# Kernel optimization log

Measured on AMD Instinct MI355X. Metric: run time of the kernel, lower is better.

The kernel has to match this reference:

```python
import jax, jax.numpy as jnp
import numpy as np

N_E = 1024     # codebook size (n_e, nbooks=1)
E_DIM = 256    # embedding dim
BETA = 0.25
B, T = 16, 4096


def setup_inputs() -> dict:
    key = jax.random.key(0)
    k1, k2 = jax.random.split(key)
    z = jax.random.normal(k1, (B, T, E_DIM), dtype=jnp.float32)
    # matches torch init: uniform(-1/n_e_i, 1/n_e_i)
    codebook = jax.random.uniform(k2, (N_E, E_DIM), dtype=jnp.float32,
                                  minval=-1.0 / N_E, maxval=1.0 / N_E)
    return {"z": z, "codebook": codebook}


def reference(z, codebook):
    zf = z.reshape(-1, E_DIM)                                   # [N, d]
    dist = (jnp.sum(zf * zf, axis=1, keepdims=True)
            - 2.0 * (zf @ codebook.T)
            + jnp.sum(codebook * codebook, axis=1)[None, :])
    idx = jnp.argmin(dist, axis=1)                              # [N]
    # one-hot scatter + matmul == codebook gather
    z_q = codebook[idx].reshape(z.shape)                        # [B, T, d]
    loss = (jnp.mean((z_q - jax.lax.stop_gradient(z)) ** 2)
            + BETA * jnp.mean((z - jax.lax.stop_gradient(z_q)) ** 2))
    # straight-through estimator
    z_q_st = z + jax.lax.stop_gradient(z_q - z)
    indices = idx.reshape(z.shape[:-1] + (1,))                  # [B, T, 1]
    return z_q_st, loss, indices
```

## Files before the change

kernel.cpp:

```cpp
#include <hip/hip_runtime.h>
#include <hip/hip_bf16.h>
#include <math.h>

typedef __bf16 bf16x8 __attribute__((ext_vector_type(8)));
typedef float f32x4 __attribute__((ext_vector_type(4)));
typedef unsigned short u16x8 __attribute__((ext_vector_type(8)));

constexpr int EDIM = 256;
constexpr int NE = 1024;
constexpr int NROWS = 65536;
constexpr float BETA = 0.25f;

constexpr size_t A2T_OFF   = 0;
constexpr size_t A2T_SZ    = (size_t)512 * 16 * 8192;
constexpr size_t B2T_OFF   = A2T_OFF + A2T_SZ;
constexpr size_t B2T_SZ    = (size_t)8 * 16 * 8192;
constexpr size_t SZROW_OFF = B2T_OFF + B2T_SZ;
constexpr size_t SZABS_OFF = SZROW_OFF + 262144;
constexpr size_t CNORM_OFF = SZABS_OFF + 262144;
constexpr size_t BMAX_OFF  = CNORM_OFF + 4096;
constexpr size_t EMAX_OFF  = BMAX_OFF + 4096;
constexpr size_t CNT_OFF   = EMAX_OFF + 256;
constexpr size_t LIST_OFF  = CNT_OFF + 256;
constexpr size_t LPART_OFF = LIST_OFF + 262144;
constexpr size_t LP2_OFF   = LPART_OFF + 262144;
constexpr size_t WS_NEED   = LP2_OFF + 1024;

__device__ __forceinline__ unsigned short f32_to_bf16_rne(float f) {
    unsigned u = __float_as_uint(f);
    u += 0x7fffu + ((u >> 16) & 1u);
    return (unsigned short)(u >> 16);
}
__device__ __forceinline__ float bf16_to_f32(unsigned short h) {
    return __uint_as_float((unsigned)h << 16);
}

#define GLL16(g, l)                                                                   \
    __builtin_amdgcn_global_load_lds(                                                 \
        (const __attribute__((address_space(1))) unsigned int*)(g),                   \
        (__attribute__((address_space(3))) unsigned int*)(l), 16, 0, 0)

__global__ __launch_bounds__(64)
void p3_codebook(const float* __restrict__ cb, float* __restrict__ cnorm,
                 char* __restrict__ B2t, float* __restrict__ bmax) {
    __shared__ float xr[256];
    __shared__ float rres[16];
    __shared__ unsigned short ehi[256], elo[256];
    const int e = blockIdx.x, l = threadIdx.x;
    const float4 v = reinterpret_cast<const float4*>(cb + (size_t)e * EDIM)[l];
    *reinterpret_cast<float4*>(&xr[l * 4]) = v;
    float amax = fmaxf(fmaxf(fabsf(v.x), fabsf(v.y)), fmaxf(fabsf(v.z), fabsf(v.w)));
    #pragma unroll
    for (int off = 32; off; off >>= 1) amax = fmaxf(amax, __shfl_down(amax, off));
    __syncthreads();
    #pragma unroll
    for (int i = 0; i < 4; ++i) {
        const int idx = i * 64 + l;
        const float f = xr[idx];
        const unsigned short h = f32_to_bf16_rne(f);
        ehi[idx] = h;
        elo[idx] = f32_to_bf16_rne(f - bf16_to_f32(h));
    }
    if (l < 16) {
        const float* x = xr + (l >> 3) * 128;
        const int j = l & 7;
        float r = __fmul_rn(x[j], x[j]);
        for (int i = 8; i < 128; i += 8) r = __fadd_rn(r, __fmul_rn(x[i + j], x[i + j]));
        rres[l] = r;
    }
    __syncthreads();
    if (l == 0) {
        float h0 = __fadd_rn(__fadd_rn(__fadd_rn(rres[0], rres[1]), __fadd_rn(rres[2], rres[3])),
                             __fadd_rn(__fadd_rn(rres[4], rres[5]), __fadd_rn(rres[6], rres[7])));
        float h1 = __fadd_rn(__fadd_rn(__fadd_rn(rres[8], rres[9]), __fadd_rn(rres[10], rres[11])),
                             __fadd_rn(__fadd_rn(rres[12], rres[13]), __fadd_rn(rres[14], rres[15])));
        cnorm[e] = __fadd_rn(h0, h1);
        bmax[e] = amax;
    }
    {
        const int c = l >> 2, kgv = l & 3;
        const int colbase = ((c < 8) ? c * 32 : (c - 8) * 32) + kgv * 8;
        const unsigned short* src = (c < 8) ? ehi : elo;
        char* dst = B2t + ((((size_t)(e >> 7) * 16 + c) * 512 + (size_t)kgv * 128 + (e & 127)) * 16);
        *reinterpret_cast<uint4*>(dst) = *reinterpret_cast<const uint4*>(&src[colbase]);
    }
}

__global__ void k_emax(const float* __restrict__ bmax, float* __restrict__ emax, int* cnt) {
    __shared__ float red[256];
    if (threadIdx.x == 0) cnt[0] = 0;
    float m = 0.f;
    for (int i = threadIdx.x; i < NE; i += 256) m = fmaxf(m, bmax[i]);
    red[threadIdx.x] = m;
    __syncthreads();
    for (int h = 128; h; h >>= 1) {
        if (threadIdx.x < h) red[threadIdx.x] = fmaxf(red[threadIdx.x], red[threadIdx.x + h]);
        __syncthreads();
    }
    if (threadIdx.x == 0) emax[0] = red[0];
}

__global__ __launch_bounds__(256)
void p2_atile(const float* __restrict__ z, char* __restrict__ A2t,
              float* __restrict__ szrow, float* __restrict__ szabs) {
    __shared__ float t[64][260];
    __shared__ float ch[64][16];
    const int mt = blockIdx.x, h = blockIdx.y, tid = threadIdx.x;
    const int row0 = mt * 128 + h * 64;
    #pragma unroll
    for (int i = 0; i < 16; ++i) {
        const int fid = i * 256 + tid;
        const int r = fid >> 6, c4 = fid & 63;
        const float4 v = *reinterpret_cast<const float4*>(
            z + (size_t)(row0 + r) * EDIM + c4 * 4);
        *reinterpret_cast<float4*>(&t[r][c4 * 4]) = v;
    }
    __syncthreads();
    {
        const int r = tid >> 2, q = tid & 3;
        float asum = 0.f;
        for (int c = 0; c < 64; ++c) asum += fabsf(t[r][q * 64 + c]);
        asum += __shfl_xor(asum, 1);
        asum += __shfl_xor(asum, 2);
        #pragma unroll
        for (int cc = 0; cc < 4; ++cc) {
            const int chain = q * 4 + cc;
            const float* x = &t[r][(chain >> 3) * 128];
            const int j = chain & 7;
            float rr = __fmul_rn(x[j], x[j]);
            for (int i = 8; i < 128; i += 8) rr = __fadd_rn(rr, __fmul_rn(x[i + j], x[i + j]));
            ch[r][chain] = rr;
        }
        __syncthreads();
        if (q == 0) {
            const float* c0 = ch[r];
            const float h0 = __fadd_rn(__fadd_rn(__fadd_rn(c0[0], c0[1]), __fadd_rn(c0[2], c0[3])),
                                       __fadd_rn(__fadd_rn(c0[4], c0[5]), __fadd_rn(c0[6], c0[7])));
            const float h1 = __fadd_rn(__fadd_rn(__fadd_rn(c0[8], c0[9]), __fadd_rn(c0[10], c0[11])),
                                       __fadd_rn(__fadd_rn(c0[12], c0[13]), __fadd_rn(c0[14], c0[15])));
            szrow[row0 + r] = __fadd_rn(h0, h1);
            szabs[row0 + r] = asum;
        }
    }
    #pragma unroll
    for (int i = 0; i < 16; ++i) {
        const int sid = i * 256 + tid;
        const int ca = sid >> 8, kgv = (sid >> 6) & 3, rwl = sid & 63;
        const int cbase = ((ca < 8) ? ca : ca - 8) * 32 + kgv * 8;
        u16x8 out;
        #pragma unroll
        for (int j = 0; j < 8; ++j) {
            const float f = t[rwl][cbase + j];
            unsigned short h16 = f32_to_bf16_rne(f);
            if (ca >= 8) h16 = f32_to_bf16_rne(f - bf16_to_f32(h16));
            out[j] = h16;
        }
        char* dst = A2t + ((((size_t)mt * 16 + ca) * 512 + (size_t)kgv * 128 + (h * 64 + rwl)) * 16);
        *reinterpret_cast<u16x8*>(dst) = out;
    }
}

__global__ __launch_bounds__(256, 1)
void vq_main(const char* __restrict__ A2t, const char* __restrict__ B2t,
             const float* __restrict__ cnorm, const float* __restrict__ szrow,
             const float* __restrict__ szabs, const float* __restrict__ emaxp,
             const float* __restrict__ cb,
             float* __restrict__ idxf, int* __restrict__ cnt, int* __restrict__ list,
             float* __restrict__ zq, float* __restrict__ lpart) {
    constexpr int CNS = 131072;
    __shared__ char smem[135168] __attribute__((aligned(16)));
    float* cns = reinterpret_cast<float*>(smem + CNS);
    float (*ms1)[2] = reinterpret_cast<float(*)[2]>(smem);
    float (*ms2)[2] = reinterpret_cast<float(*)[2]>(smem + 1024);
    int   (*mi1)[2] = reinterpret_cast<int(*)[2]>(smem + 2048);
    int*  bidx      = reinterpret_cast<int*>(smem + 3072);

    const int tid = threadIdx.x;
    const int mtile = blockIdx.x;
    const size_t rowbase = (size_t)mtile * 128;
    const int l = tid & 63, wid = tid >> 6;
    const int kg = l >> 4, li = l & 15;
    const int wr = wid >> 1, wc = wid & 1;

    GLL16((const char*)cnorm + tid * 16, smem + CNS + tid * 16);
    const char* Ag = A2t + (size_t)mtile * 131072;
    #pragma unroll
    for (int i = 0; i < 32; ++i)
        GLL16(Ag + (i * 256 + tid) * 16, smem + (i * 256 + tid) * 16);
    asm volatile("s_waitcnt vmcnt(0)" ::: "memory");
    __syncthreads();

    int aoff[4], boff[4];
    #pragma unroll
    for (int f = 0; f < 4; ++f) {
        aoff[f] = kg * 2048 + (wr * 64 + f * 16 + li) * 16;
        boff[f] = kg * 2048 + (wc * 64 + f * 16 + li) * 16;
    }

    bf16x8 cAh[4], cAl[4], cB[4];
    #pragma unroll
    for (int f = 0; f < 4; ++f) {
        cAh[f] = *reinterpret_cast<const bf16x8*>(smem + 0 * 8192 + aoff[f]);
        cAl[f] = *reinterpret_cast<const bf16x8*>(smem + 8 * 8192 + aoff[f]);
        cB[f]  = *reinterpret_cast<const bf16x8*>(B2t + boff[f]);
    }

    float s1v[4][4], s2v[4][4];
    int i1v[4][4];
    #pragma unroll
    for (int a = 0; a < 4; ++a)
        #pragma unroll
        for (int b = 0; b < 4; ++b) { s1v[a][b] = 3.4e38f; s2v[a][b] = 3.4e38f; i1v[a][b] = 0; }

    for (int nt = 0; nt < 8; ++nt) {
        f32x4 acc[4][4];
        const f32x4 zf4 = {0.f, 0.f, 0.f, 0.f};
        #pragma unroll
        for (int a = 0; a < 4; ++a)
            #pragma unroll
            for (int b = 0; b < 4; ++b) acc[a][b] = zf4;

        #pragma unroll
        for (int j = 0; j < 16; ++j) {
            const int g = nt * 16 + j;
            bf16x8 nAh[4], nAl[4], nB[4];
            {
                const int jn = (j + 1) & 15;
                const char* gB = B2t + (size_t)(g + 1) * 8192;
                #pragma unroll
                for (int f = 0; f < 4; ++f)
                    nB[f] = *reinterpret_cast<const bf16x8*>(gB + boff[f]);
                if (jn < 8) {
                    #pragma unroll
                    for (int f = 0; f < 4; ++f) {
                        nAh[f] = *reinterpret_cast<const bf16x8*>(smem + jn * 8192 + aoff[f]);
                        nAl[f] = *reinterpret_cast<const bf16x8*>(smem + (8 + jn) * 8192 + aoff[f]);
                    }
                } else {
                    #pragma unroll
                    for (int f = 0; f < 4; ++f) {
                        nAh[f] = *reinterpret_cast<const bf16x8*>(smem + (jn - 8) * 8192 + aoff[f]);
                        nAl[f] = cAl[f];
                    }
                }
            }
            #pragma unroll
            for (int fm = 0; fm < 4; ++fm)
                #pragma unroll
                for (int fn = 0; fn < 4; ++fn)
                    acc[fm][fn] = __builtin_amdgcn_mfma_f32_16x16x32_bf16(cAh[fm], cB[fn], acc[fm][fn], 0, 0, 0);
            if (j < 8) {
                #pragma unroll
                for (int fm = 0; fm < 4; ++fm)
                    #pragma unroll
                    for (int fn = 0; fn < 4; ++fn)
                        acc[fm][fn] = __builtin_amdgcn_mfma_f32_16x16x32_bf16(cAl[fm], cB[fn], acc[fm][fn], 0, 0, 0);
            }
            #pragma unroll
            for (int f = 0; f < 4; ++f) { cAh[f] = nAh[f]; cAl[f] = nAl[f]; cB[f] = nB[f]; }
        }

        const int ntb = nt * 128;
        #pragma unroll
        for (int fn = 0; fn < 4; ++fn) {
            const int e = ntb + wc * 64 + fn * 16 + li;
            const float cn = cns[e];
            #pragma unroll
            for (int fm = 0; fm < 4; ++fm)
                #pragma unroll
                for (int r = 0; r < 4; ++r) {
                    const float s = cn - 2.0f * acc[fm][fn][r];
                    if (s < s1v[fm][r]) { s2v[fm][r] = s1v[fm][r]; s1v[fm][r] = s; i1v[fm][r] = e; }
                    else s2v[fm][r] = fminf(s2v[fm][r], s);
                }
        }
    }

    __syncthreads();

    #pragma unroll
    for (int fm = 0; fm < 4; ++fm)
        #pragma unroll
        for (int r = 0; r < 4; ++r) {
            float s1 = s1v[fm][r], s2 = s2v[fm][r];
            int i1 = i1v[fm][r];
            #pragma unroll
            for (int off = 1; off < 16; off <<= 1) {
                const float os1 = __shfl_xor(s1, off);
                const float os2 = __shfl_xor(s2, off);
                const int oi1 = __shfl_xor(i1, off);
                const bool take = (os1 < s1) || (os1 == s1 && oi1 < i1);
                const float loser = take ? s1 : os1;
                if (take) { s1 = os1; i1 = oi1; }
                s2 = fminf(fminf(s2, os2), loser);
            }
            if (li == 0) {
                const int rloc = wr * 64 + fm * 16 + (kg << 2) + r;
                ms1[rloc][wc] = s1; ms2[rloc][wc] = s2; mi1[rloc][wc] = i1;
            }
        }
    __syncthreads();

    if (tid < 128) {
        const float a1 = ms1[tid][0], b1 = ms1[tid][1];
        const float a2 = ms2[tid][0], b2 = ms2[tid][1];
        const int ai = mi1[tid][0], bi = mi1[tid][1];
        const bool take = (b1 < a1) || (b1 == a1 && bi < ai);
        const float s1 = take ? b1 : a1;
        const int i1 = take ? bi : ai;
        const float loser = take ? a1 : b1;
        const float s2 = fminf(fminf(a2, b2), loser);
        const int rowg = (int)rowbase + tid;
        const float szv = szrow[rowg], sab = szabs[rowg];
        const float M = 2.0e-4f * sab * emaxp[0] + ldexpf(1.0f, ilogbf(szv * 1.02f) - 23);
        idxf[rowg] = (float)i1;
        lpart[rowg] = s1 + szv;
        bidx[tid] = i1;
        if (s2 - s1 <= 2.0f * M) { const int p = atomicAdd(cnt, 1); list[p] = rowg; }
    }
    __syncthreads();

    {
        const float4* cb4 = reinterpret_cast<const float4*>(cb);
        float4* zq4 = reinterpret_cast<float4*>(zq);
        #pragma unroll 4
        for (int j = 0; j < 32; ++j) {
            const int rr = wid * 32 + j;
            const int e = bidx[rr];
            zq4[(rowbase + rr) * 64 + l] = cb4[(size_t)e * 64 + l];
        }
    }
}

__global__ __launch_bounds__(256)
void vq_rescan(const float* __restrict__ z, const float* __restrict__ cb,
               const float* __restrict__ cnorm, const float* __restrict__ szrow,
               const int* __restrict__ list, const int* __restrict__ cntp,
               float* __restrict__ idxf, float* __restrict__ zq, float* __restrict__ lpart) {
    __shared__ float zr[8][260];
    __shared__ float szs[8];
    __shared__ int rows_s[8];
    __shared__ float sred[256];
    __shared__ int ired[256];
    const int tid = threadIdx.x;
    const int n = cntp[0];
    const int groups = (n + 7) >> 3;
    for (int g = blockIdx.x; g < groups; g += gridDim.x) {
        if (tid < 8) {
            const int gi = g * 8 + tid;
            const int row = (gi < n) ? list[gi] : -1;
            rows_s[tid] = row;
            szs[tid] = (row >= 0) ? szrow[row] : 0.f;
        }
        __syncthreads();
        #pragma unroll
        for (int i = 0; i < 8; ++i) {
            const int sid = i * 256 + tid;
            const int rr = sid >> 8, k = sid & 255;
            if (rows_s[rr] >= 0) zr[rr][k] = z[(size_t)rows_s[rr] * EDIM + k];
        }
        __syncthreads();
        float bs[8];
        int bi[8];
        #pragma unroll
        for (int rr = 0; rr < 8; ++rr) { bs[rr] = 3.4e38f; bi[rr] = 0; }
        for (int q = 0; q < 4; ++q) {
            const int e = tid + q * 256;
            const float4* crow = reinterpret_cast<const float4*>(cb + (size_t)e * EDIM);
            float d[8];
            #pragma unroll
            for (int rr = 0; rr < 8; ++rr) d[rr] = 0.f;
            for (int k4 = 0; k4 < 64; ++k4) {
                const float4 c4 = crow[k4];
                #pragma unroll
                for (int rr = 0; rr < 8; ++rr) {
                    d[rr] = fmaf(zr[rr][k4 * 4 + 0], c4.x, d[rr]);
                    d[rr] = fmaf(zr[rr][k4 * 4 + 1], c4.y, d[rr]);
                    d[rr] = fmaf(zr[rr][k4 * 4 + 2], c4.z, d[rr]);
                    d[rr] = fmaf(zr[rr][k4 * 4 + 3], c4.w, d[rr]);
                }
            }
            const float cn = cnorm[e];
            #pragma unroll
            for (int rr = 0; rr < 8; ++rr) {
                const float b1 = __fadd_rn(szs[rr], __fmul_rn(-2.0f, d[rr]));
                const float s = __fadd_rn(b1, cn);
                if (s < bs[rr]) { bs[rr] = s; bi[rr] = e; }
            }
        }
        #pragma unroll
        for (int rr = 0; rr < 8; ++rr) {
            sred[tid] = bs[rr];
            ired[tid] = bi[rr];
            __syncthreads();
            for (int h = 128; h; h >>= 1) {
                if (tid < h) {
                    const float so = sred[tid + h];
                    const int io = ired[tid + h];
                    if (so < sred[tid] || (so == sred[tid] && io < ired[tid])) {
                        sred[tid] = so; ired[tid] = io;
                    }
                }
                __syncthreads();
            }
            if (rows_s[rr] >= 0) {
                const int best = ired[0];
                const int row = rows_s[rr];
                zq[(size_t)row * EDIM + tid] = cb[(size_t)best * EDIM + tid];
                if (tid == 0) { idxf[row] = (float)best; lpart[row] = sred[0]; }
            }
            __syncthreads();
        }
    }
}

__global__ void vq_loss1(const float* __restrict__ lpart, float* __restrict__ lp2) {
    __shared__ float red[256];
    const int t = threadIdx.x;
    red[t] = lpart[blockIdx.x * 256 + t];
    __syncthreads();
    for (int h = 128; h; h >>= 1) {
        if (t < h) red[t] += red[t + h];
        __syncthreads();
    }
    if (t == 0) lp2[blockIdx.x] = red[0];
}
__global__ void vq_loss2(const float* __restrict__ lp2, float* __restrict__ outloss) {
    __shared__ float red[256];
    const int t = threadIdx.x;
    red[t] = lp2[t];
    __syncthreads();
    for (int h = 128; h; h >>= 1) {
        if (t < h) red[t] += red[t + h];
        __syncthreads();
    }
    if (t == 0) outloss[0] = red[0] * ((1.0f + BETA) / 16777216.0f);
}

__device__ __forceinline__ float np_sum128_sq(const float* __restrict__ x) {
    float r[8];
    #pragma unroll
    for (int j = 0; j < 8; ++j) r[j] = __fmul_rn(x[j], x[j]);
    #pragma unroll
    for (int i = 8; i < 128; i += 8)
        #pragma unroll
        for (int j = 0; j < 8; ++j) r[j] = __fadd_rn(r[j], __fmul_rn(x[i + j], x[i + j]));
    return __fadd_rn(__fadd_rn(__fadd_rn(r[0], r[1]), __fadd_rn(r[2], r[3])),
                     __fadd_rn(__fadd_rn(r[4], r[5]), __fadd_rn(r[6], r[7])));
}
__global__ void fb_prep(const float* __restrict__ z, const float* __restrict__ cb,
                        float* __restrict__ szrow, float* __restrict__ cnorm) {
    int t = blockIdx.x * blockDim.x + threadIdx.x;
    if (t < NROWS) {
        const float* x = z + (size_t)t * EDIM;
        szrow[t] = __fadd_rn(np_sum128_sq(x), np_sum128_sq(x + 128));
    } else if (t < NROWS + NE) {
        const float* x = cb + (size_t)(t - NROWS) * EDIM;
        cnorm[t - NROWS] = __fadd_rn(np_sum128_sq(x), np_sum128_sq(x + 128));
    }
}
__global__ __launch_bounds__(256, 2)
void fb_vq(const float* __restrict__ z, const float* __restrict__ cb,
           const float* __restrict__ cnorm, const float* __restrict__ szrow,
           float* __restrict__ zq, float* __restrict__ idxf, float* __restrict__ lpart) {
    __shared__ float As[64 * 268];
    __shared__ float Bs[32 * 68];
    __shared__ int bidx[64];
    __shared__ float lred[4];
    const int tid = threadIdx.x;
    const int tx = tid & 15, ty = tid >> 4;
    const size_t rowbase = (size_t)blockIdx.x * 64;
    const float4* zg = reinterpret_cast<const float4*>(z + rowbase * EDIM);
    #pragma unroll
    for (int it = 0; it < 16; ++it) {
        int id = it * 256 + tid;
        int r = id >> 6, c4 = id & 63;
        float4 v = zg[id];
        *reinterpret_cast<float4*>(&As[r * 268 + c4 * 4]) = v;
    }
    float sz[4];
    #pragma unroll
    for (int m = 0; m < 4; ++m) sz[m] = szrow[rowbase + ty * 4 + m];
    float bestS[4]; int bestI[4];
    #pragma unroll
    for (int m = 0; m < 4; ++m) { bestS[m] = 3.4e38f; bestI[m] = 0; }
    for (int nt = 0; nt < NE / 64; ++nt) {
        float acc[4][4];
        #pragma unroll
        for (int m = 0; m < 4; ++m)
            #pragma unroll
            for (int n = 0; n < 4; ++n) acc[m][n] = 0.f;
        const int ebase = nt * 64;
        for (int k0 = 0; k0 < EDIM; k0 += 32) {
            __syncthreads();
            #pragma unroll
            for (int i = 0; i < 8; ++i) {
                int id = i * 256 + tid;
                int n = id >> 5, k = id & 31;
                Bs[k * 68 + n] = cb[(size_t)(ebase + n) * EDIM + k0 + k];
            }
            __syncthreads();
            #pragma unroll
            for (int kg2 = 0; kg2 < 32; kg2 += 4) {
                float4 a[4], b[4];
                #pragma unroll
                for (int m = 0; m < 4; ++m)
                    a[m] = *reinterpret_cast<const float4*>(&As[(ty * 4 + m) * 268 + k0 + kg2]);
                #pragma unroll
                for (int kk = 0; kk < 4; ++kk)
                    b[kk] = *reinterpret_cast<const float4*>(&Bs[(kg2 + kk) * 68 + tx * 4]);
                #pragma unroll
                for (int m = 0; m < 4; ++m) {
                    const float* av = reinterpret_cast<const float*>(&a[m]);
                    #pragma unroll
                    for (int kk = 0; kk < 4; ++kk) {
                        acc[m][0] = fmaf(av[kk], b[kk].x, acc[m][0]);
                        acc[m][1] = fmaf(av[kk], b[kk].y, acc[m][1]);
                        acc[m][2] = fmaf(av[kk], b[kk].z, acc[m][2]);
                        acc[m][3] = fmaf(av[kk], b[kk].w, acc[m][3]);
                    }
                }
            }
        }
        #pragma unroll
        for (int n = 0; n < 4; ++n) {
            int e = ebase + tx * 4 + n;
            float cn = cnorm[e];
            #pragma unroll
            for (int m = 0; m < 4; ++m) {
                float b1 = __fadd_rn(sz[m], __fmul_rn(-2.0f, acc[m][n]));
                float s = __fadd_rn(b1, cn);
                if (s < bestS[m]) { bestS[m] = s; bestI[m] = e; }
            }
        }
    }
    #pragma unroll
    for (int m = 0; m < 4; ++m) {
        float s = bestS[m]; int i = bestI[m];
        #pragma unroll
        for (int off = 1; off < 16; off <<= 1) {
            float s2 = __shfl_xor(s, off);
            int i2 = __shfl_xor(i, off);
            if (s2 < s || (s2 == s && i2 < i)) { s = s2; i = i2; }
        }
        if (tx == 0) bidx[ty * 4 + m] = i;
    }
    __syncthreads();
    if (tid < 64) idxf[rowbase + tid] = (float)bidx[tid];
    float lsum = 0.f;
    for (int r = 0; r < 64; ++r) {
        int e = bidx[r];
        float c = cb[(size_t)e * EDIM + tid];
        float zv = As[r * 268 + tid];
        float d = c - zv;
        lsum = fmaf(d, d, lsum);
        zq[(rowbase + r) * EDIM + tid] = c;
    }
    #pragma unroll
    for (int off = 32; off; off >>= 1) lsum += __shfl_down(lsum, off);
    if ((tid & 63) == 0) lred[tid >> 6] = lsum;
    __syncthreads();
    if (tid == 0) lpart[blockIdx.x] = lred[0] + lred[1] + lred[2] + lred[3];
}
__global__ void fb_loss(const float* __restrict__ lpart, float* __restrict__ out_loss) {
    __shared__ float red[256];
    int tid = threadIdx.x;
    float s = 0.f;
    for (int i = tid; i < NROWS / 64; i += 256) s += lpart[i];
    red[tid] = s;
    __syncthreads();
    for (int h = 128; h; h >>= 1) {
        if (tid < h) red[tid] += red[tid + h];
        __syncthreads();
    }
    if (tid == 0) out_loss[0] = red[0] * (1.0f + BETA) / (float)((size_t)NROWS * EDIM);
}

extern "C" void kernel_launch(void* const* d_in, const int* in_sizes, int n_in,
                              void* d_out, int out_size, void* d_ws, size_t ws_size,
                              hipStream_t stream) {
    const float* z = (const float*)d_in[0];
    const float* cb = (const float*)d_in[1];
    float* out = (float*)d_out;
    float* zq = out;
    float* loss = out + (size_t)NROWS * EDIM;
    float* idxf = loss + 1;
    char* ws = (char*)d_ws;

    if (ws_size < WS_NEED) {
        float* cnorm = (float*)ws;
        float* szrow = cnorm + NE;
        float* lpart = szrow + NROWS;
        hipLaunchKernelGGL(fb_prep, dim3((NROWS + NE + 255) / 256), dim3(256), 0, stream, z, cb, szrow, cnorm);
        hipLaunchKernelGGL(fb_vq, dim3(NROWS / 64), dim3(256), 0, stream, z, cb, cnorm, szrow, zq, idxf, lpart);
        hipLaunchKernelGGL(fb_loss, dim3(1), dim3(256), 0, stream, lpart, loss);
        return;
    }

    char* A2t = ws + A2T_OFF;
    char* B2t = ws + B2T_OFF;
    float* szrow = (float*)(ws + SZROW_OFF);
    float* szabs = (float*)(ws + SZABS_OFF);
    float* cnorm = (float*)(ws + CNORM_OFF);
    float* bmax = (float*)(ws + BMAX_OFF);
    float* emax = (float*)(ws + EMAX_OFF);
    int* cnt = (int*)(ws + CNT_OFF);
    int* list = (int*)(ws + LIST_OFF);
    float* lpart = (float*)(ws + LPART_OFF);
    float* lp2 = (float*)(ws + LP2_OFF);

    hipLaunchKernelGGL(p3_codebook, dim3(NE), dim3(64), 0, stream, cb, cnorm, B2t, bmax);
    hipLaunchKernelGGL(k_emax, dim3(1), dim3(256), 0, stream, bmax, emax, cnt);
    hipLaunchKernelGGL(p2_atile, dim3(512, 2), dim3(256), 0, stream, z, A2t, szrow, szabs);
    hipLaunchKernelGGL(vq_main, dim3(512), dim3(256), 0, stream,
                       A2t, B2t, cnorm, szrow, szabs, emax, cb, idxf, cnt, list, zq, lpart);
    hipLaunchKernelGGL(vq_rescan, dim3(1024), dim3(256), 0, stream,
                       z, cb, cnorm, szrow, list, cnt, idxf, zq, lpart);
    hipLaunchKernelGGL(vq_loss1, dim3(256), dim3(256), 0, stream, lpart, lp2);
    hipLaunchKernelGGL(vq_loss2, dim3(1), dim3(256), 0, stream, lp2, loss);
}
```

Measured before the change: 243.0 us.

## Split vq_main work across eight waves instead of four

The main distance kernel now runs 512 threads per block. Waves are arranged 2x4, each covering 32 codebook columns instead of 64, which halves per-wave accumulators and B-fragment loads. The cross-wave argmin merge now reduces over four column groups. The goal is more waves per CU to hide latency, since LDS (~132KB) caps it at one block per CU. The cost is duplicated A-fragment LDS reads across more waves and a larger merge step. launch_bounds(512,2) asks for two blocks per CU, which the LDS size likely cannot provide.

```diff
diff --git a/kernel.cpp b/kernel.cpp
--- a/kernel.cpp
+++ b/kernel.cpp
@@ -160,7 +160,7 @@
     }
 }
 
-__global__ __launch_bounds__(256, 1)
+__global__ __launch_bounds__(512, 2)
 void vq_main(const char* __restrict__ A2t, const char* __restrict__ B2t,
              const float* __restrict__ cnorm, const float* __restrict__ szrow,
              const float* __restrict__ szabs, const float* __restrict__ emaxp,
@@ -170,40 +170,43 @@
     constexpr int CNS = 131072;
     __shared__ char smem[135168] __attribute__((aligned(16)));
     float* cns = reinterpret_cast<float*>(smem + CNS);
-    float (*ms1)[2] = reinterpret_cast<float(*)[2]>(smem);
-    float (*ms2)[2] = reinterpret_cast<float(*)[2]>(smem + 1024);
-    int   (*mi1)[2] = reinterpret_cast<int(*)[2]>(smem + 2048);
-    int*  bidx      = reinterpret_cast<int*>(smem + 3072);
+    float (*ms1)[4] = reinterpret_cast<float(*)[4]>(smem);
+    float (*ms2)[4] = reinterpret_cast<float(*)[4]>(smem + 2048);
+    int   (*mi1)[4] = reinterpret_cast<int(*)[4]>(smem + 4096);
+    int*  bidx      = reinterpret_cast<int*>(smem + 6144);
 
     const int tid = threadIdx.x;
     const int mtile = blockIdx.x;
     const size_t rowbase = (size_t)mtile * 128;
     const int l = tid & 63, wid = tid >> 6;
     const int kg = l >> 4, li = l & 15;
-    const int wr = wid >> 1, wc = wid & 1;
-
-    GLL16((const char*)cnorm + tid * 16, smem + CNS + tid * 16);
+    const int wr = wid >> 2, wc = wid & 3;
+
+    if (tid < 256) GLL16((const char*)cnorm + tid * 16, smem + CNS + tid * 16);
     const char* Ag = A2t + (size_t)mtile * 131072;
     #pragma unroll
-    for (int i = 0; i < 32; ++i)
-        GLL16(Ag + (i * 256 + tid) * 16, smem + (i * 256 + tid) * 16);
+    for (int i = 0; i < 16; ++i)
+        GLL16(Ag + (i * 512 + tid) * 16, smem + (i * 512 + tid) * 16);
     asm volatile("s_waitcnt vmcnt(0)" ::: "memory");
     __syncthreads();
 
-    int aoff[4], boff[4];
-    #pragma unroll
-    for (int f = 0; f < 4; ++f) {
+    int aoff[4], boff[2];
+    #pragma unroll
+    for (int f = 0; f < 4; ++f)
         aoff[f] = kg * 2048 + (wr * 64 + f * 16 + li) * 16;
-        boff[f] = kg * 2048 + (wc * 64 + f * 16 + li) * 16;
-    }
-
-    bf16x8 cAh[4], cAl[4], cB[4];
+    #pragma unroll
+    for (int f = 0; f < 2; ++f)
+        boff[f] = kg * 2048 + (wc * 32 + f * 16 + li) * 16;
+
+    bf16x8 cAh[4], cAl[4], cB[2];
     #pragma unroll
     for (int f = 0; f < 4; ++f) {
         cAh[f] = *reinterpret_cast<const bf16x8*>(smem + 0 * 8192 + aoff[f]);
         cAl[f] = *reinterpret_cast<const bf16x8*>(smem + 8 * 8192 + aoff[f]);
-        cB[f]  = *reinterpret_cast<const bf16x8*>(B2t + boff[f]);
-    }
+    }
+    #pragma unroll
+    for (int f = 0; f < 2; ++f)
+        cB[f] = *reinterpret_cast<const bf16x8*>(B2t + boff[f]);
 
     float s1v[4][4], s2v[4][4];
     int i1v[4][4];
@@ -213,22 +216,22 @@
         for (int b = 0; b < 4; ++b) { s1v[a][b] = 3.4e38f; s2v[a][b] = 3.4e38f; i1v[a][b] = 0; }
 
     for (int nt = 0; nt < 8; ++nt) {
-        f32x4 acc[4][4];
+        f32x4 acc[4][2];
         const f32x4 zf4 = {0.f, 0.f, 0.f, 0.f};
         #pragma unroll
         for (int a = 0; a < 4; ++a)
             #pragma unroll
-            for (int b = 0; b < 4; ++b) acc[a][b] = zf4;
+            for (int b = 0; b < 2; ++b) acc[a][b] = zf4;
 
         #pragma unroll
         for (int j = 0; j < 16; ++j) {
             const int g = nt * 16 + j;
-            bf16x8 nAh[4], nAl[4], nB[4];
+            bf16x8 nAh[4], nAl[4], nB[2];
             {
                 const int jn = (j + 1) & 15;
                 const char* gB = B2t + (size_t)(g + 1) * 8192;
                 #pragma unroll
-                for (int f = 0; f < 4; ++f)
+                for (int f = 0; f < 2; ++f)
                     nB[f] = *reinterpret_cast<const bf16x8*>(gB + boff[f]);
                 if (jn < 8) {
                     #pragma unroll
@@ -247,23 +250,25 @@
             #pragma unroll
             for (int fm = 0; fm < 4; ++fm)
                 #pragma unroll
-                for (int fn = 0; fn < 4; ++fn)
+                for (int fn = 0; fn < 2; ++fn)
                     acc[fm][fn] = __builtin_amdgcn_mfma_f32_16x16x32_bf16(cAh[fm], cB[fn], acc[fm][fn], 0, 0, 0);
             if (j < 8) {
                 #pragma unroll
                 for (int fm = 0; fm < 4; ++fm)
                     #pragma unroll
-                    for (int fn = 0; fn < 4; ++fn)
+                    for (int fn = 0; fn < 2; ++fn)
                         acc[fm][fn] = __builtin_amdgcn_mfma_f32_16x16x32_bf16(cAl[fm], cB[fn], acc[fm][fn], 0, 0, 0);
             }
             #pragma unroll
-            for (int f = 0; f < 4; ++f) { cAh[f] = nAh[f]; cAl[f] = nAl[f]; cB[f] = nB[f]; }
+            for (int f = 0; f < 4; ++f) { cAh[f] = nAh[f]; cAl[f] = nAl[f]; }
+            #pragma unroll
+            for (int f = 0; f < 2; ++f) cB[f] = nB[f];
         }
 
         const int ntb = nt * 128;
         #pragma unroll
-        for (int fn = 0; fn < 4; ++fn) {
-            const int e = ntb + wc * 64 + fn * 16 + li;
+        for (int fn = 0; fn < 2; ++fn) {
+            const int e = ntb + wc * 32 + fn * 16 + li;
             const float cn = cns[e];
             #pragma unroll
             for (int fm = 0; fm < 4; ++fm)
@@ -302,14 +307,17 @@
     __syncthreads();
 
     if (tid < 128) {
-        const float a1 = ms1[tid][0], b1 = ms1[tid][1];
-        const float a2 = ms2[tid][0], b2 = ms2[tid][1];
-        const int ai = mi1[tid][0], bi = mi1[tid][1];
-        const bool take = (b1 < a1) || (b1 == a1 && bi < ai);
-        const float s1 = take ? b1 : a1;
-        const int i1 = take ? bi : ai;
-        const float loser = take ? a1 : b1;
-        const float s2 = fminf(fminf(a2, b2), loser);
+        float s1 = ms1[tid][0], s2 = ms2[tid][0];
+        int i1 = mi1[tid][0];
+        #pragma unroll
+        for (int q = 1; q < 4; ++q) {
+            const float o1 = ms1[tid][q], o2 = ms2[tid][q];
+            const int oi = mi1[tid][q];
+            const bool take = (o1 < s1) || (o1 == s1 && oi < i1);
+            const float loser = take ? s1 : o1;
+            if (take) { s1 = o1; i1 = oi; }
+            s2 = fminf(fminf(s2, o2), loser);
+        }
         const int rowg = (int)rowbase + tid;
         const float szv = szrow[rowg], sab = szabs[rowg];
         const float M = 2.0e-4f * sab * emaxp[0] + ldexpf(1.0f, ilogbf(szv * 1.02f) - 23);
@@ -324,8 +332,8 @@
         const float4* cb4 = reinterpret_cast<const float4*>(cb);
         float4* zq4 = reinterpret_cast<float4*>(zq);
         #pragma unroll 4
-        for (int j = 0; j < 32; ++j) {
-            const int rr = wid * 32 + j;
+        for (int j = 0; j < 16; ++j) {
+            const int rr = wid * 16 + j;
             const int e = bidx[rr];
             zq4[(rowbase + rr) * 64 + l] = cb4[(size_t)e * 64 + l];
         }
@@ -612,7 +620,7 @@
     hipLaunchKernelGGL(p3_codebook, dim3(NE), dim3(64), 0, stream, cb, cnorm, B2t, bmax);
     hipLaunchKernelGGL(k_emax, dim3(1), dim3(256), 0, stream, bmax, emax, cnt);
     hipLaunchKernelGGL(p2_atile, dim3(512, 2), dim3(256), 0, stream, z, A2t, szrow, szabs);
-    hipLaunchKernelGGL(vq_main, dim3(512), dim3(256), 0, stream,
+    hipLaunchKernelGGL(vq_main, dim3(512), dim3(512), 0, stream,
                        A2t, B2t, cnorm, szrow, szabs, emax, cb, idxf, cnt, list, zq, lpart);
     hipLaunchKernelGGL(vq_rescan, dim3(1024), dim3(256), 0, stream,
                        z, cb, cnorm, szrow, list, cnt, idxf, zq, lpart);
```

Result: slower. 378.9 us (+56.0%).
